# Kernel tuning notes

Measured on AMD Instinct MI355X. Metric: run time of the kernel, lower is better.

Reference implementation:

```python
import jax, jax.numpy as jnp
import numpy as np

N_NODES = 50000
N_EDGES = 800000
IN_F, HID, OUT_F = 128, 128, 64


def setup_inputs() -> dict:
    key = jax.random.key(0)
    k1, k2, k3, k4 = jax.random.split(key, 4)
    x = jax.random.normal(k1, (N_NODES, IN_F), dtype=jnp.float32)
    edge_index = jax.random.randint(k2, (2, N_EDGES), 0, N_NODES, dtype=jnp.int64)
    # Glorot-style scaled weights, zero bias (PyG GCNConv default)
    W1 = jax.random.normal(k3, (IN_F, HID), dtype=jnp.float32) * (1.0 / np.sqrt(IN_F))
    b1 = jnp.zeros((HID,), dtype=jnp.float32)
    W2 = jax.random.normal(k4, (HID, OUT_F), dtype=jnp.float32) * (1.0 / np.sqrt(HID))
    b2 = jnp.zeros((OUT_F,), dtype=jnp.float32)
    return {"x": x, "edge_index": edge_index, "W1": W1, "b1": b1, "W2": W2, "b2": b2}


def reference(x, edge_index, W1, b1, W2, b2):
    n = x.shape[0]
    # add self-loops (PyG GCNConv default add_self_loops=True)
    loop = jnp.arange(n, dtype=edge_index.dtype)
    src = jnp.concatenate([edge_index[0], loop])  # message source nodes
    dst = jnp.concatenate([edge_index[1], loop])  # aggregation target nodes
    # symmetric normalization: D^{-1/2} (A+I) D^{-1/2}
    deg = jax.ops.segment_sum(jnp.ones(dst.shape, dtype=x.dtype), dst, num_segments=n)
    dinv = jnp.where(deg > 0, jax.lax.rsqrt(deg), 0.0)
    norm = dinv[src] * dinv[dst]  # [E+N]

    def gcn_conv(h, W, b):
        h = h @ W                              # dense transform first (PyG order)
        msg = h[src] * norm[:, None]           # gather + scale: [E+N, d]
        agg = jax.ops.segment_sum(msg, dst, num_segments=n)  # scatter-add
        return agg + b

    h = jax.nn.relu(gcn_conv(x, W1, b1))
    return gcn_conv(h, W2, b2)
```

## Files before the change

### kernel.cpp

```cpp
#include <hip/hip_runtime.h>
#include <hip/hip_bf16.h>

#define NN   50000
#define NE   800000
#define F_IN 128
#define F_H  128
#define F_O  64

#define BINSHIFT 7
#define NBINS    ((NN + 127) >> 7)
#define CAP      2816
#define EPB      2048

static constexpr int NB_G1 = (NN + 63) / 64;

typedef __bf16 bf16_8 __attribute__((ext_vector_type(8)));
typedef float  f32x4  __attribute__((ext_vector_type(4)));

template <typename AT, int K, int NOUT, bool SCALE>
__device__ __forceinline__ void gemm_body(const AT* __restrict__ X,
                                          const float* __restrict__ W,
                                          const float* __restrict__ dinv,
                                          __hip_bfloat16* __restrict__ Y,
                                          __hip_bfloat16* WB, int blk) {
    constexpr int NKS = K / 32;
    constexpr int NC  = NOUT / 16;
    const int t = threadIdx.x;
    for (int f = t; f < K * NOUT; f += 256) {
        int k = f / NOUT, n = f % NOUT;
        int ks = k >> 5, kr = k & 31, qq = kr >> 3, jj = kr & 7;
        int c = n >> 4, nn = n & 15;
        WB[(((ks * NC + c) * 16 + nn) * 4 + qq) * 8 + jj] = __float2bfloat16(W[f]);
    }
    __syncthreads();

    const int wave = t >> 6, lane = t & 63;
    const int r = lane & 15, q = lane >> 4;
    const int m0 = blk * 64 + wave * 16;
    int arow = m0 + r;
    if (arow >= NN) arow = NN - 1;

    f32x4 acc[NC];
#pragma unroll
    for (int c = 0; c < NC; ++c) acc[c] = (f32x4){0.f, 0.f, 0.f, 0.f};

#pragma unroll
    for (int ks = 0; ks < NKS; ++ks) {
        bf16_8 a;
        if constexpr (sizeof(AT) == 4) {
            const float* xp = (const float*)X + (size_t)arow * K + ks * 32 + q * 8;
            float4 x0 = ((const float4*)xp)[0];
            float4 x1 = ((const float4*)xp)[1];
            a[0] = (__bf16)x0.x; a[1] = (__bf16)x0.y; a[2] = (__bf16)x0.z; a[3] = (__bf16)x0.w;
            a[4] = (__bf16)x1.x; a[5] = (__bf16)x1.y; a[6] = (__bf16)x1.z; a[7] = (__bf16)x1.w;
        } else {
            a = *(const bf16_8*)((const __hip_bfloat16*)X + (size_t)arow * K + ks * 32 + q * 8);
        }
#pragma unroll
        for (int c = 0; c < NC; ++c) {
            bf16_8 b = *(const bf16_8*)&WB[(((ks * NC + c) * 16 + r) * 4 + q) * 8];
            acc[c] = __builtin_amdgcn_mfma_f32_16x16x32_bf16(a, b, acc[c], 0, 0, 0);
        }
    }

#pragma unroll
    for (int c = 0; c < NC; ++c) {
#pragma unroll
        for (int i = 0; i < 4; ++i) {
            int gr = m0 + q * 4 + i;
            if (gr < NN) {
                float v = acc[c][i];
                if constexpr (SCALE) v *= dinv[gr];
                Y[(size_t)gr * NOUT + c * 16 + r] = __float2bfloat16(v);
            }
        }
    }
}

__global__ __launch_bounds__(256) void k_fuseA(const float* __restrict__ X,
                                               const float* __restrict__ W1,
                                               __hip_bfloat16* __restrict__ Xw,
                                               const int* __restrict__ ei32,
                                               int* __restrict__ binbuf,
                                               unsigned* __restrict__ bincnt) {
    __shared__ __align__(16) char smem[32768];
    const int t = threadIdx.x;

    if (blockIdx.x < NB_G1) {
        gemm_body<float, F_IN, F_H, false>(X, W1, nullptr, Xw,
                                           (__hip_bfloat16*)smem, blockIdx.x);
        return;
    }

    unsigned* hist = (unsigned*)smem;
    unsigned* base = hist + NBINS;
    unsigned* rank = base + NBINS;
    for (int i = t; i < NBINS; i += 256) { hist[i] = 0u; rank[i] = 0u; }
    __syncthreads();

    const bool is64 = ((ei32[1] | ei32[3] | ei32[5] | ei32[7]) == 0);
    const int e0 = (blockIdx.x - NB_G1) * EPB;
    int pk[8], bin[8];
#pragma unroll
    for (int j = 0; j < 8; ++j) {
        int e = e0 + t + j * 256;
        if (e < NE) {
            int s, d;
            if (is64) {
                const long long* p = (const long long*)ei32;
                s = (int)p[e];
                d = (int)p[NE + e];
            } else {
                s = ei32[e];
                d = ei32[NE + e];
            }
            pk[j]  = (s << BINSHIFT) | (d & 127);
            bin[j] = d >> BINSHIFT;
        } else bin[j] = -1;
    }
#pragma unroll
    for (int j = 0; j < 8; ++j)
        if (bin[j] >= 0) atomicAdd(&hist[bin[j]], 1u);
    __syncthreads();
    for (int b = t; b < NBINS; b += 256)
        base[b] = atomicAdd(&bincnt[b], hist[b]);
    __syncthreads();
#pragma unroll
    for (int j = 0; j < 8; ++j) {
        if (bin[j] >= 0) {
            unsigned rk = atomicAdd(&rank[bin[j]], 1u);
            binbuf[(size_t)bin[j] * CAP + base[bin[j]] + rk] = pk[j];
        }
    }
}

__global__ __launch_bounds__(512) void k_binscan(const unsigned* __restrict__ bincnt,
                                                 unsigned* __restrict__ bscan) {
    __shared__ unsigned s[512];
    const int t = threadIdx.x;
    unsigned v = (t < NBINS) ? bincnt[t] : 0u;
    s[t] = v;
    __syncthreads();
    for (int off = 1; off < 512; off <<= 1) {
        unsigned u = (t >= off) ? s[t - off] : 0u;
        __syncthreads();
        s[t] += u;
        __syncthreads();
    }
    if (t < NBINS) bscan[t] = s[t] - v;
}

__global__ __launch_bounds__(256) void k_phaseB(const int* __restrict__ binbuf,
                                                const unsigned* __restrict__ bincnt,
                                                const unsigned* __restrict__ bscan,
                                                unsigned* __restrict__ row_ptr,
                                                float* __restrict__ dinv,
                                                int* __restrict__ srcs) {
    __shared__ unsigned h[128];
    __shared__ unsigned cur[128];
    const int b = blockIdx.x, t = threadIdx.x;
    if (t < 128) h[t] = 0u;
    __syncthreads();
    const unsigned n = bincnt[b];
    const int* buf = binbuf + (size_t)b * CAP;
    for (unsigned i = t; i < n; i += 256)
        atomicAdd(&h[buf[i] & 127], 1u);
    __syncthreads();
    if (t < 128) cur[t] = h[t];
    __syncthreads();
    for (int off = 1; off < 128; off <<= 1) {
        unsigned u = (t < 128 && t >= off) ? cur[t - off] : 0u;
        __syncthreads();
        if (t < 128) cur[t] += u;
        __syncthreads();
    }
    if (t < 128) {
        unsigned ex = bscan[b] + cur[t] - h[t];
        int node = (b << BINSHIFT) + t;
        if (node < NN) {
            row_ptr[node] = ex;
            dinv[node]    = rsqrtf((float)(h[t] + 1u));
        }
        cur[t] = ex;
    }
    if (b == NBINS - 1 && t == 0) row_ptr[NN] = NE;
    __syncthreads();
    for (unsigned i = t; i < n; i += 256) {
        int p = buf[i];
        unsigned pos = atomicAdd(&cur[p & 127], 1u);
        srcs[pos] = p >> BINSHIFT;
    }
}

__global__ __launch_bounds__(256) void k_agg1(const __hip_bfloat16* __restrict__ Xw,
                                              const int* __restrict__ srcs,
                                              const unsigned* __restrict__ row_ptr,
                                              const float* __restrict__ dinv,
                                              const float* __restrict__ b1,
                                              __hip_bfloat16* __restrict__ H) {
    const int wv   = (blockIdx.x * 256 + threadIdx.x) >> 6;
    const int lane = threadIdx.x & 63;
    if (wv >= NN) return;
    const int sub = lane >> 4;
    const int fl  = lane & 15;
    const float dn = dinv[wv];

    float acc[8];
    bf16_8 self = *(const bf16_8*)(Xw + (size_t)wv * F_H + fl * 8);
    const float sw = (sub == 0) ? dn : 0.f;
#pragma unroll
    for (int j = 0; j < 8; ++j) acc[j] = sw * (float)self[j];

    const unsigned ie = row_ptr[wv + 1];
    for (unsigned i = row_ptr[wv] + sub; i < ie; i += 4) {
        int s = srcs[i];
        float dsc = dinv[s];
        bf16_8 row = *(const bf16_8*)(Xw + (size_t)s * F_H + fl * 8);
#pragma unroll
        for (int j = 0; j < 8; ++j) acc[j] += dsc * (float)row[j];
    }
#pragma unroll
    for (int j = 0; j < 8; ++j) {
        acc[j] += __shfl_xor(acc[j], 16, 64);
        acc[j] += __shfl_xor(acc[j], 32, 64);
    }
    if (sub == 0) {
        bf16_8 o;
#pragma unroll
        for (int j = 0; j < 8; ++j) {
            float v = fmaxf(dn * acc[j] + b1[fl * 8 + j], 0.f);
            o[j] = (__bf16)v;
        }
        *(bf16_8*)(H + (size_t)wv * F_H + fl * 8) = o;
    }
}

__global__ __launch_bounds__(256) void k_gemm2(const __hip_bfloat16* __restrict__ H1,
                                               const float* __restrict__ W2,
                                               const float* __restrict__ dinv,
                                               __hip_bfloat16* __restrict__ Hw) {
    __shared__ __align__(16) __hip_bfloat16 WB[(F_H / 32) * (F_O / 16) * 512];
    gemm_body<__hip_bfloat16, F_H, F_O, true>(H1, W2, dinv, Hw, WB, blockIdx.x);
}

__global__ __launch_bounds__(256) void k_agg2(const __hip_bfloat16* __restrict__ Hw,
                                              const int* __restrict__ srcs,
                                              const unsigned* __restrict__ row_ptr,
                                              const float* __restrict__ dinv,
                                              const float* __restrict__ b2,
                                              float* __restrict__ out) {
    const int wv   = (blockIdx.x * 256 + threadIdx.x) >> 6;
    const int lane = threadIdx.x & 63;
    if (wv >= NN) return;
    const int sub = lane >> 3;
    const int fl  = lane & 7;

    float acc[8];
    bf16_8 self = *(const bf16_8*)(Hw + (size_t)wv * F_O + fl * 8);
#pragma unroll
    for (int j = 0; j < 8; ++j) acc[j] = (sub == 0) ? (float)self[j] : 0.f;

    const unsigned ie = row_ptr[wv + 1];
    for (unsigned i = row_ptr[wv] + sub; i < ie; i += 8) {
        int s = srcs[i];
        bf16_8 row = *(const bf16_8*)(Hw + (size_t)s * F_O + fl * 8);
#pragma unroll
        for (int j = 0; j < 8; ++j) acc[j] += (float)row[j];
    }
#pragma unroll
    for (int j = 0; j < 8; ++j) {
        acc[j] += __shfl_xor(acc[j], 8, 64);
        acc[j] += __shfl_xor(acc[j], 16, 64);
        acc[j] += __shfl_xor(acc[j], 32, 64);
    }
    if (sub == 0) {
        float dn = dinv[wv];
        float4 o0 = make_float4(dn * acc[0] + b2[fl * 8 + 0], dn * acc[1] + b2[fl * 8 + 1],
                                dn * acc[2] + b2[fl * 8 + 2], dn * acc[3] + b2[fl * 8 + 3]);
        float4 o1 = make_float4(dn * acc[4] + b2[fl * 8 + 4], dn * acc[5] + b2[fl * 8 + 5],
                                dn * acc[6] + b2[fl * 8 + 6], dn * acc[7] + b2[fl * 8 + 7]);
        float4* op = (float4*)(out + (size_t)wv * F_O + fl * 8);
        op[0] = o0;
        op[1] = o1;
    }
}

extern "C" void kernel_launch(void* const* d_in, const int* in_sizes, int n_in,
                              void* d_out, int out_size, void* d_ws, size_t ws_size,
                              hipStream_t stream) {
    const float* x  = (const float*)d_in[0];
    const int*   ei = (const int*)d_in[1];
    const float* W1 = (const float*)d_in[2];
    const float* b1 = (const float*)d_in[3];
    const float* W2 = (const float*)d_in[4];
    const float* b2 = (const float*)d_in[5];
    float* out = (float*)d_out;

    char* w = (char*)d_ws;
    size_t off = 0;
    auto alloc = [&](size_t bytes) {
        void* p = w + off;
        off += (bytes + 255) & ~(size_t)255;
        return p;
    };
    unsigned* row_ptr = (unsigned*)alloc((size_t)(NN + 1) * 4);
    float*    dinv    = (float*)alloc((size_t)NN * 4);
    unsigned* bincnt  = (unsigned*)alloc((size_t)NBINS * 4);
    unsigned* bscan   = (unsigned*)alloc((size_t)NBINS * 4);
    int*      srcs    = (int*)alloc((size_t)NE * 4);
    int*      binbuf  = (int*)alloc((size_t)NBINS * CAP * 4);
    __hip_bfloat16* Xw = (__hip_bfloat16*)alloc((size_t)NN * F_H * 2);
    __hip_bfloat16* H1 = (__hip_bfloat16*)alloc((size_t)NN * F_H * 2);
    __hip_bfloat16* Hw = Xw;

    const int NB_BIN = (NE + EPB - 1) / EPB;

    hipMemsetAsync(bincnt, 0, (size_t)NBINS * 4, stream);
    k_fuseA<<<NB_G1 + NB_BIN, 256, 0, stream>>>(x, W1, Xw, ei, binbuf, bincnt);
    k_binscan<<<1, 512, 0, stream>>>(bincnt, bscan);
    k_phaseB<<<NBINS, 256, 0, stream>>>(binbuf, bincnt, bscan, row_ptr, dinv, srcs);

    k_agg1<<<(NN + 3) / 4, 256, 0, stream>>>(Xw, srcs, row_ptr, dinv, b1, H1);
    k_gemm2<<<(NN + 63) / 64, 256, 0, stream>>>(H1, W2, dinv, Hw);
    k_agg2<<<(NN + 3) / 4, 256, 0, stream>>>(Hw, srcs, row_ptr, dinv, b2, out);
}
```

Measured before the change: 192.5 us.

## Fold bin scan into phaseB, reorder fused blocks, dual-accumulate aggregation loops

Removes the single-block k_binscan launch; each phaseB block now computes its own global base by summing the preceding bin counts with a block reduction. The fused kernel now places edge-binning blocks ahead of GEMM1 blocks, so the atomics-heavy binning is dispatched first. Both aggregation kernels process two neighbors per iteration into separate accumulators to raise memory-level parallelism. The cost is redundant bin-count reads per phaseB block and somewhat higher register use.

```diff
diff --git a/kernel.cpp b/kernel.cpp
--- a/kernel.cpp
+++ b/kernel.cpp
@@ -12,7 +12,8 @@
 #define CAP      2816
 #define EPB      2048
 
-static constexpr int NB_G1 = (NN + 63) / 64;
+static constexpr int NB_G1  = (NN + 63) / 64;
+static constexpr int NB_BIN = (NE + EPB - 1) / EPB;
 
 typedef __bf16 bf16_8 __attribute__((ext_vector_type(8)));
 typedef float  f32x4  __attribute__((ext_vector_type(4)));
@@ -86,9 +87,10 @@
     __shared__ __align__(16) char smem[32768];
     const int t = threadIdx.x;
 
-    if (blockIdx.x < NB_G1) {
+    if (blockIdx.x >= NB_BIN) {
         gemm_body<float, F_IN, F_H, false>(X, W1, nullptr, Xw,
-                                           (__hip_bfloat16*)smem, blockIdx.x);
+                                           (__hip_bfloat16*)smem,
+                                           blockIdx.x - NB_BIN);
         return;
     }
 
@@ -99,7 +101,7 @@
     __syncthreads();
 
     const bool is64 = ((ei32[1] | ei32[3] | ei32[5] | ei32[7]) == 0);
-    const int e0 = (blockIdx.x - NB_G1) * EPB;
+    const int e0 = blockIdx.x * EPB;
     int pk[8], bin[8];
 #pragma unroll
     for (int j = 0; j < 8; ++j) {
@@ -134,33 +136,28 @@
     }
 }
 
-__global__ __launch_bounds__(512) void k_binscan(const unsigned* __restrict__ bincnt,
-                                                 unsigned* __restrict__ bscan) {
-    __shared__ unsigned s[512];
-    const int t = threadIdx.x;
-    unsigned v = (t < NBINS) ? bincnt[t] : 0u;
-    s[t] = v;
-    __syncthreads();
-    for (int off = 1; off < 512; off <<= 1) {
-        unsigned u = (t >= off) ? s[t - off] : 0u;
-        __syncthreads();
-        s[t] += u;
-        __syncthreads();
-    }
-    if (t < NBINS) bscan[t] = s[t] - v;
-}
-
 __global__ __launch_bounds__(256) void k_phaseB(const int* __restrict__ binbuf,
                                                 const unsigned* __restrict__ bincnt,
-                                                const unsigned* __restrict__ bscan,
                                                 unsigned* __restrict__ row_ptr,
                                                 float* __restrict__ dinv,
                                                 int* __restrict__ srcs) {
     __shared__ unsigned h[128];
     __shared__ unsigned cur[128];
+    __shared__ unsigned red[256];
     const int b = blockIdx.x, t = threadIdx.x;
+
+    unsigned part = 0;
+    for (int i = t; i < NBINS; i += 256)
+        if (i < b) part += bincnt[i];
+    red[t] = part;
     if (t < 128) h[t] = 0u;
     __syncthreads();
+    for (int off = 128; off > 0; off >>= 1) {
+        if (t < off) red[t] += red[t + off];
+        __syncthreads();
+    }
+    const unsigned gbase = red[0];
+
     const unsigned n = bincnt[b];
     const int* buf = binbuf + (size_t)b * CAP;
     for (unsigned i = t; i < n; i += 256)
@@ -175,7 +172,7 @@
         __syncthreads();
     }
     if (t < 128) {
-        unsigned ex = bscan[b] + cur[t] - h[t];
+        unsigned ex = gbase + cur[t] - h[t];
         int node = (b << BINSHIFT) + t;
         if (node < NN) {
             row_ptr[node] = ex;
@@ -205,30 +202,44 @@
     const int fl  = lane & 15;
     const float dn = dinv[wv];
 
-    float acc[8];
+    float acc0[8], acc1[8];
     bf16_8 self = *(const bf16_8*)(Xw + (size_t)wv * F_H + fl * 8);
     const float sw = (sub == 0) ? dn : 0.f;
 #pragma unroll
-    for (int j = 0; j < 8; ++j) acc[j] = sw * (float)self[j];
+    for (int j = 0; j < 8; ++j) { acc0[j] = sw * (float)self[j]; acc1[j] = 0.f; }
 
     const unsigned ie = row_ptr[wv + 1];
-    for (unsigned i = row_ptr[wv] + sub; i < ie; i += 4) {
+    unsigned i = row_ptr[wv] + sub;
+    for (; i + 4 < ie; i += 8) {
+        int s0 = srcs[i], s1 = srcs[i + 4];
+        float d0 = dinv[s0], d1 = dinv[s1];
+        bf16_8 r0 = *(const bf16_8*)(Xw + (size_t)s0 * F_H + fl * 8);
+        bf16_8 r1 = *(const bf16_8*)(Xw + (size_t)s1 * F_H + fl * 8);
+#pragma unroll
+        for (int j = 0; j < 8; ++j) {
+            acc0[j] += d0 * (float)r0[j];
+            acc1[j] += d1 * (float)r1[j];
+        }
+    }
+    if (i < ie) {
         int s = srcs[i];
-        float dsc = dinv[s];
-        bf16_8 row = *(const bf16_8*)(Xw + (size_t)s * F_H + fl * 8);
-#pragma unroll
-        for (int j = 0; j < 8; ++j) acc[j] += dsc * (float)row[j];
-    }
-#pragma unroll
-    for (int j = 0; j < 8; ++j) {
-        acc[j] += __shfl_xor(acc[j], 16, 64);
-        acc[j] += __shfl_xor(acc[j], 32, 64);
+        float d = dinv[s];
+        bf16_8 r = *(const bf16_8*)(Xw + (size_t)s * F_H + fl * 8);
+#pragma unroll
+        for (int j = 0; j < 8; ++j) acc0[j] += d * (float)r[j];
+    }
+#pragma unroll
+    for (int j = 0; j < 8; ++j) {
+        float a = acc0[j] + acc1[j];
+        a += __shfl_xor(a, 16, 64);
+        a += __shfl_xor(a, 32, 64);
+        acc0[j] = a;
     }
     if (sub == 0) {
         bf16_8 o;
 #pragma unroll
         for (int j = 0; j < 8; ++j) {
-            float v = fmaxf(dn * acc[j] + b1[fl * 8 + j], 0.f);
+            float v = fmaxf(dn * acc0[j] + b1[fl * 8 + j], 0.f);
             o[j] = (__bf16)v;
         }
         *(bf16_8*)(H + (size_t)wv * F_H + fl * 8) = o;
@@ -255,30 +266,46 @@
     const int sub = lane >> 3;
     const int fl  = lane & 7;
 
-    float acc[8];
+    float acc0[8], acc1[8];
     bf16_8 self = *(const bf16_8*)(Hw + (size_t)wv * F_O + fl * 8);
 #pragma unroll
-    for (int j = 0; j < 8; ++j) acc[j] = (sub == 0) ? (float)self[j] : 0.f;
+    for (int j = 0; j < 8; ++j) {
+        acc0[j] = (sub == 0) ? (float)self[j] : 0.f;
+        acc1[j] = 0.f;
+    }
 
     const unsigned ie = row_ptr[wv + 1];
-    for (unsigned i = row_ptr[wv] + sub; i < ie; i += 8) {
+    unsigned i = row_ptr[wv] + sub;
+    for (; i + 8 < ie; i += 16) {
+        int s0 = srcs[i], s1 = srcs[i + 8];
+        bf16_8 r0 = *(const bf16_8*)(Hw + (size_t)s0 * F_O + fl * 8);
+        bf16_8 r1 = *(const bf16_8*)(Hw + (size_t)s1 * F_O + fl * 8);
+#pragma unroll
+        for (int j = 0; j < 8; ++j) {
+            acc0[j] += (float)r0[j];
+            acc1[j] += (float)r1[j];
+        }
+    }
+    if (i < ie) {
         int s = srcs[i];
-        bf16_8 row = *(const bf16_8*)(Hw + (size_t)s * F_O + fl * 8);
-#pragma unroll
-        for (int j = 0; j < 8; ++j) acc[j] += (float)row[j];
-    }
-#pragma unroll
-    for (int j = 0; j < 8; ++j) {
-        acc[j] += __shfl_xor(acc[j], 8, 64);
-        acc[j] += __shfl_xor(acc[j], 16, 64);
-        acc[j] += __shfl_xor(acc[j], 32, 64);
+        bf16_8 r = *(const bf16_8*)(Hw + (size_t)s * F_O + fl * 8);
+#pragma unroll
+        for (int j = 0; j < 8; ++j) acc0[j] += (float)r[j];
+    }
+#pragma unroll
+    for (int j = 0; j < 8; ++j) {
+        float a = acc0[j] + acc1[j];
+        a += __shfl_xor(a, 8, 64);
+        a += __shfl_xor(a, 16, 64);
+        a += __shfl_xor(a, 32, 64);
+        acc0[j] = a;
     }
     if (sub == 0) {
         float dn = dinv[wv];
-        float4 o0 = make_float4(dn * acc[0] + b2[fl * 8 + 0], dn * acc[1] + b2[fl * 8 + 1],
-                                dn * acc[2] + b2[fl * 8 + 2], dn * acc[3] + b2[fl * 8 + 3]);
-        float4 o1 = make_float4(dn * acc[4] + b2[fl * 8 + 4], dn * acc[5] + b2[fl * 8 + 5],
-                                dn * acc[6] + b2[fl * 8 + 6], dn * acc[7] + b2[fl * 8 + 7]);
+        float4 o0 = make_float4(dn * acc0[0] + b2[fl * 8 + 0], dn * acc0[1] + b2[fl * 8 + 1],
+                                dn * acc0[2] + b2[fl * 8 + 2], dn * acc0[3] + b2[fl * 8 + 3]);
+        float4 o1 = make_float4(dn * acc0[4] + b2[fl * 8 + 4], dn * acc0[5] + b2[fl * 8 + 5],
+                                dn * acc0[6] + b2[fl * 8 + 6], dn * acc0[7] + b2[fl * 8 + 7]);
         float4* op = (float4*)(out + (size_t)wv * F_O + fl * 8);
         op[0] = o0;
         op[1] = o1;
@@ -306,19 +333,15 @@
     unsigned* row_ptr = (unsigned*)alloc((size_t)(NN + 1) * 4);
     float*    dinv    = (float*)alloc((size_t)NN * 4);
     unsigned* bincnt  = (unsigned*)alloc((size_t)NBINS * 4);
-    unsigned* bscan   = (unsigned*)alloc((size_t)NBINS * 4);
     int*      srcs    = (int*)alloc((size_t)NE * 4);
     int*      binbuf  = (int*)alloc((size_t)NBINS * CAP * 4);
     __hip_bfloat16* Xw = (__hip_bfloat16*)alloc((size_t)NN * F_H * 2);
     __hip_bfloat16* H1 = (__hip_bfloat16*)alloc((size_t)NN * F_H * 2);
     __hip_bfloat16* Hw = Xw;
 
-    const int NB_BIN = (NE + EPB - 1) / EPB;
-
     hipMemsetAsync(bincnt, 0, (size_t)NBINS * 4, stream);
-    k_fuseA<<<NB_G1 + NB_BIN, 256, 0, stream>>>(x, W1, Xw, ei, binbuf, bincnt);
-    k_binscan<<<1, 512, 0, stream>>>(bincnt, bscan);
-    k_phaseB<<<NBINS, 256, 0, stream>>>(binbuf, bincnt, bscan, row_ptr, dinv, srcs);
+    k_fuseA<<<NB_BIN + NB_G1, 256, 0, stream>>>(x, W1, Xw, ei, binbuf, bincnt);
+    k_phaseB<<<NBINS, 256, 0, stream>>>(binbuf, bincnt, row_ptr, dinv, srcs);
 
     k_agg1<<<(NN + 3) / 4, 256, 0, stream>>>(Xw, srcs, row_ptr, dinv, b1, H1);
     k_gemm2<<<(NN + 63) / 64, 256, 0, stream>>>(H1, W2, dinv, Hw);
```

Measured after the change: 192.1 us. Within noise of the previous version (-0.2%).
